# Performance work log

Measured on AMD Instinct MI355X. Metric: run time of the kernel, lower is better.

The kernel has to match this reference:

```python
import jax, jax.numpy as jnp
import numpy as np

N_WAY = 64

def setup_inputs() -> dict:
    key = jax.random.key(0)
    k1, k2, k3, k4 = jax.random.split(key, 4)
    S, Q, F, D = 1024, 16384, 2048, 512
    xs = jax.random.normal(k1, (S, F), dtype=jnp.float32)
    ys = jax.random.randint(k2, (S,), 0, N_WAY, dtype=jnp.int64)
    xq = jax.random.normal(k3, (Q, F), dtype=jnp.float32)
    W = jax.random.normal(k4, (F, D), dtype=jnp.float32) * 0.02
    b = jnp.zeros((D,), dtype=jnp.float32)
    return {"xs": xs, "ys": ys, "xq": xq, "W": W, "b": b}

def reference(xs, ys, xq, W, b):
    # encoder: linear projection [*, F] -> [*, D]
    z_s = xs @ W + b            # [S, D]
    z_q = xq @ W + b            # [Q, D]
    # class prototypes: segment mean over support embeddings -> [N_way, D]
    counts = jax.ops.segment_sum(jnp.ones_like(ys, dtype=z_s.dtype), ys, num_segments=N_WAY)
    proto = jax.ops.segment_sum(z_s, ys, num_segments=N_WAY) / jnp.clip(counts, 1.0)[:, None]
    # pairwise squared euclidean distance (expand + pow + sum), [Q, N_way]
    diff = z_q[:, None, :] - proto[None, :, :]   # [Q, N_way, D]
    dists = jnp.sum(diff * diff, axis=-1)
    return -dists
```

## Files before the change

### kernel.cpp

```cpp
#include <hip/hip_runtime.h>


typedef __attribute__((ext_vector_type(8))) short short8;
typedef __attribute__((ext_vector_type(4))) float floatx4;

#define S_ROWS 1024
#define F_DIM  2048
#define D_DIM  512
#define NWAY   64
#define Q_ROWS 16384
#define ZS_LD  136

static __device__ __forceinline__ unsigned short f2bf(float f) {
  unsigned int u = __float_as_uint(f);
  u += 0x7FFF + ((u >> 16) & 1);
  return (unsigned short)(u >> 16);
}
static __device__ __forceinline__ float bf2f(unsigned short s) {
  return __uint_as_float(((unsigned int)s) << 16);
}
static __device__ __forceinline__ unsigned int pack_bf2(float x, float y) {
  unsigned int ux = __float_as_uint(x) + 0x8000u;
  unsigned int uy = __float_as_uint(y) + 0x8000u;
  return __builtin_amdgcn_perm(uy, ux, 0x07060302u);
}
static __device__ __forceinline__ void load_lds16(const unsigned short* g, unsigned short* l) {
  __builtin_amdgcn_global_load_lds((const __attribute__((address_space(1))) unsigned int*)g,
                                   (__attribute__((address_space(3))) unsigned int*)l,
                                   16, 0, 0);
}

__global__ __launch_bounds__(256) void k_prep(const float* __restrict__ W,
                                              unsigned short* __restrict__ Wt,
                                              float* __restrict__ outz,
                                              float* __restrict__ pnorm_part,
                                              const int* __restrict__ ys,
                                              int* __restrict__ order,
                                              int* __restrict__ starts,
                                              float* __restrict__ counts) {
  __shared__ unsigned short t[64][65];
  __shared__ int cnt[NWAY];
  __shared__ int st[NWAY + 1];
  __shared__ int wp[NWAY];
  int bx = blockIdx.x;
  int tid = threadIdx.x;
  if (bx < 256) {
    float4 zz = {0.f, 0.f, 0.f, 0.f};
#pragma unroll
    for (int p = 0; p < 4; p++)
      *(float4*)&outz[(size_t)bx * 4096 + p * 1024 + tid * 4] = zz;
    int f0 = (bx >> 3) << 6;
    int d0 = (bx & 7) << 6;
    for (int j = 0; j < 16; j++) {
      int lin = j * 256 + tid;
      int fl = lin >> 6, dl = lin & 63;
      t[fl][dl] = f2bf(W[(size_t)(f0 + fl) * D_DIM + d0 + dl]);
    }
    __syncthreads();
    for (int j = 0; j < 16; j++) {
      int lin = j * 256 + tid;
      int dl = lin >> 6, fl = lin & 63;
      Wt[(size_t)(d0 + dl) * F_DIM + f0 + fl] = t[fl][dl];
    }
  } else {
    pnorm_part[tid] = 0.f;
    if (tid < NWAY) cnt[tid] = 0;
    __syncthreads();
    for (int j = tid; j < S_ROWS; j += 256) atomicAdd(&cnt[ys[j]], 1);
    __syncthreads();
    if (tid == 0) {
      int a = 0;
      for (int c = 0; c < NWAY; c++) { st[c] = a; wp[c] = a; a += cnt[c]; }
      st[NWAY] = a;
    }
    __syncthreads();
    for (int j = tid; j < S_ROWS; j += 256) {
      int c = ys[j];
      int p = atomicAdd(&wp[c], 1);
      order[p] = j;
    }
    if (tid < NWAY) counts[tid] = (float)cnt[tid];
    if (tid < NWAY + 1) starts[tid] = st[tid];
  }
}

__global__ __launch_bounds__(256) void k1_csum(const float* __restrict__ xs,
                                               const int* __restrict__ order,
                                               const int* __restrict__ starts,
                                               float* __restrict__ csum) {
  __shared__ int lord[S_ROWS];
  int c = blockIdx.x >> 1;
  int tid = threadIdx.x;
  int s = starts[c], e = starts[c + 1];
  int len = e - s;
  for (int j = tid; j < len; j += 256) lord[j] = order[s + j];
  __syncthreads();
  int f0 = (blockIdx.x & 1) * 1024 + tid * 4;
  float4 a = {0.f, 0.f, 0.f, 0.f};
  for (int i = 0; i < len; i++) {
    float4 v = *(const float4*)&xs[(size_t)lord[i] * F_DIM + f0];
    a.x += v.x; a.y += v.y; a.z += v.z; a.w += v.w;
  }
  *(float4*)&csum[(size_t)c * F_DIM + f0] = a;
}

__global__ __launch_bounds__(256) void k2_full(const float* __restrict__ W,
                                               const float* __restrict__ csum,
                                               const float* __restrict__ b,
                                               const float* __restrict__ counts,
                                               unsigned short* __restrict__ proto_bf,
                                               float* __restrict__ pnorm_part) {
  __shared__ __align__(16) float wch[64 * 64];
  __shared__ float csl[8 * 64];
  int bx = blockIdx.x;
  int cg = bx >> 3, dc = bx & 7;
  int c0 = cg * 8, d0 = dc * 64;
  int tid = threadIdx.x;
  int cl = tid >> 5;
  int dl = (tid & 31) * 2;
  float a0 = 0.f, a1 = 0.f;
  for (int fs = 0; fs < 32; fs++) {
    int f0 = fs * 64;
    __syncthreads();
    for (int idx = tid; idx < 4096; idx += 256) {
      int r = idx >> 6, q = idx & 63;
      wch[idx] = W[(size_t)(f0 + r) * D_DIM + d0 + q];
    }
    for (int idx = tid; idx < 512; idx += 256) {
      int r = idx >> 6, q = idx & 63;
      csl[idx] = csum[(size_t)(c0 + r) * F_DIM + f0 + q];
    }
    __syncthreads();
#pragma unroll 8
    for (int f = 0; f < 64; f++) {
      float s = csl[cl * 64 + f];
      a0 += s * wch[f * 64 + dl];
      a1 += s * wch[f * 64 + dl + 1];
    }
  }
  int c = c0 + cl;
  float cntv = counts[c];
  float inv = 1.f / fmaxf(cntv, 1.f);
  float p0 = (a0 + cntv * b[d0 + dl]) * inv;
  float p1 = (a1 + cntv * b[d0 + dl + 1]) * inv;
  unsigned short h0 = f2bf(p0), h1 = f2bf(p1);
  proto_bf[(size_t)c * D_DIM + d0 + dl] = h0;
  proto_bf[(size_t)c * D_DIM + d0 + dl + 1] = h1;
  float q0 = bf2f(h0), q1 = bf2f(h1);
  float s2 = q0 * q0 + q1 * q1;
  s2 += __shfl_xor(s2, 1, 32);
  s2 += __shfl_xor(s2, 2, 32);
  s2 += __shfl_xor(s2, 4, 32);
  s2 += __shfl_xor(s2, 8, 32);
  s2 += __shfl_xor(s2, 16, 32);
  if ((tid & 31) == 0) atomicAdd(&pnorm_part[(dc >> 1) * 64 + c], s2);
}

__global__ __launch_bounds__(256) void k3_fused(const float* __restrict__ xq,
                                                const unsigned short* __restrict__ Wt,
                                                const float* __restrict__ b,
                                                const unsigned short* __restrict__ proto_bf,
                                                const float* __restrict__ pnorm_part,
                                                float* __restrict__ out) {
  __shared__ __align__(16) char smem[66304];
  unsigned short* lA0 = (unsigned short*)smem;
  unsigned short* lB0 = (unsigned short*)(smem + 16384);
  unsigned short* lA1 = (unsigned short*)(smem + 32768);
  unsigned short* lB1 = (unsigned short*)(smem + 49152);
  unsigned short* zs = (unsigned short*)smem;
  float* qnf = (float*)(smem + 65536);
  float* pnl = (float*)(smem + 66048);

  int tid = threadIdx.x;
  int bx = blockIdx.x;
  int xcd = bx & 7;
  int wg = xcd * 64 + (bx >> 3);
  int mt = wg >> 2;
  int slice = wg & 3;
  int n0 = slice * 128;

  int wave = tid >> 6, lane = tid & 63;
  int wr = wave >> 1, wc = wave & 1;
  int lrow = lane & 15, lquad = lane >> 4;

  const float* Ab = xq + (size_t)mt * 128 * F_DIM;

  floatx4 acc[4][4];
#pragma unroll
  for (int i = 0; i < 4; i++)
#pragma unroll
    for (int j = 0; j < 4; j++) acc[i][j] = (floatx4){0.f, 0.f, 0.f, 0.f};

  int sr = tid >> 3, skq = tid & 7;
  const float* ag = Ab + (size_t)sr * F_DIM + skq * 8;
  const unsigned short* bg = Wt + (size_t)(n0 + sr) * F_DIM + skq * 8;

  float4 pf[4][2];

  auto stageB = [&](unsigned short* lBbuf, int k0) {
#pragma unroll
    for (int i = 0; i < 4; i++)
      load_lds16(bg + (size_t)i * 32 * F_DIM + k0, &lBbuf[(i * 256 + wave * 64) * 8]);
  };
  auto issueA = [&](int k0) {
#pragma unroll
    for (int p = 0; p < 4; p++) {
      const float* gp = ag + (size_t)p * 32 * F_DIM + k0;
      pf[p][0] = *(const float4*)gp;
      pf[p][1] = *(const float4*)(gp + 4);
    }
  };
  auto writeA = [&](unsigned short* lAbuf) {
#pragma unroll
    for (int p = 0; p < 4; p++) {
      uint4 w;
      w.x = pack_bf2(pf[p][0].x, pf[p][0].y);
      w.y = pack_bf2(pf[p][0].z, pf[p][0].w);
      w.z = pack_bf2(pf[p][1].x, pf[p][1].y);
      w.w = pack_bf2(pf[p][1].z, pf[p][1].w);
      *(uint4*)&lAbuf[(p * 256 + tid) * 8] = w;
    }
  };
  auto compute = [&](const unsigned short* lAbuf, const unsigned short* lBbuf) {
#pragma unroll
    for (int s = 0; s < 2; s++) {
      short8 af[4], bfr[4];
#pragma unroll
      for (int i = 0; i < 4; i++)
        af[i] = *(const short8*)&lAbuf[(wr * 64 + i * 16 + lrow) * 64 + s * 32 + lquad * 8];
#pragma unroll
      for (int j = 0; j < 4; j++)
        bfr[j] = *(const short8*)&lBbuf[(wc * 64 + j * 16 + lrow) * 64 + s * 32 + lquad * 8];
#pragma unroll
      for (int i = 0; i < 4; i++)
#pragma unroll
        for (int j = 0; j < 4; j++)
          acc[i][j] = __builtin_amdgcn_mfma_f32_16x16x32_bf16(af[i], bfr[j], acc[i][j], 0, 0, 0);
    }
  };

  stageB(lB0, 0);
  issueA(0);
  writeA(lA0);
  __syncthreads();

  for (int t = 0; t < 32; t += 2) {
    {
      int kn = (t + 1) * 64;
      stageB(lB1, kn);
      issueA(kn);
      compute(lA0, lB0);
      writeA(lA1);
      __syncthreads();
    }
    {
      if (t + 2 < 32) {
        int kn = (t + 2) * 64;
        stageB(lB0, kn);
        issueA(kn);
      }
      compute(lA1, lB1);
      if (t + 2 < 32) writeA(lA0);
      __syncthreads();
    }
  }

  if (tid < 128) qnf[tid] = 0.f;
  if (tid < 64) pnl[tid] = pnorm_part[slice * 64 + tid];
  __syncthreads();

#pragma unroll
  for (int i = 0; i < 4; i++) {
    float rn[4] = {0.f, 0.f, 0.f, 0.f};
#pragma unroll
    for (int j = 0; j < 4; j++) {
      int col = wc * 64 + j * 16 + lrow;
      float bb = b[n0 + col];
#pragma unroll
      for (int r = 0; r < 4; r++) {
        int row = wr * 64 + i * 16 + lquad * 4 + r;
        float v = acc[i][j][r] + bb;
        unsigned short h = f2bf(v);
        zs[row * ZS_LD + col] = h;
        float vq = bf2f(h);
        rn[r] += vq * vq;
      }
    }
#pragma unroll
    for (int r = 0; r < 4; r++) {
      float s2 = rn[r];
      s2 += __shfl_xor(s2, 1, 16);
      s2 += __shfl_xor(s2, 2, 16);
      s2 += __shfl_xor(s2, 4, 16);
      s2 += __shfl_xor(s2, 8, 16);
      if (lrow == 0) atomicAdd(&qnf[wr * 64 + i * 16 + lquad * 4 + r], s2);
    }
  }
  __syncthreads();

  floatx4 acc2[2][4];
#pragma unroll
  for (int i = 0; i < 2; i++)
#pragma unroll
    for (int j = 0; j < 4; j++) acc2[i][j] = (floatx4){0.f, 0.f, 0.f, 0.f};

#pragma unroll
  for (int ks = 0; ks < 4; ks++) {
    short8 af2[2], bp[4];
#pragma unroll
    for (int i = 0; i < 2; i++)
      af2[i] = *(const short8*)&zs[(wave * 32 + i * 16 + lrow) * ZS_LD + ks * 32 + lquad * 8];
#pragma unroll
    for (int j = 0; j < 4; j++)
      bp[j] = *(const short8*)&proto_bf[(size_t)(j * 16 + lrow) * D_DIM + n0 + ks * 32 + lquad * 8];
#pragma unroll
    for (int i = 0; i < 2; i++)
#pragma unroll
      for (int j = 0; j < 4; j++)
        acc2[i][j] = __builtin_amdgcn_mfma_f32_16x16x32_bf16(af2[i], bp[j], acc2[i][j], 0, 0, 0);
  }

  size_t qbase = (size_t)mt * 128;
#pragma unroll
  for (int i = 0; i < 2; i++) {
#pragma unroll
    for (int j = 0; j < 4; j++) {
      int c = j * 16 + lrow;
      float pn = pnl[c];
#pragma unroll
      for (int r = 0; r < 4; r++) {
        int ql = wave * 32 + i * 16 + lquad * 4 + r;
        float val = 2.f * acc2[i][j][r] - qnf[ql] - pn;
        atomicAdd(&out[(qbase + ql) * NWAY + c], val);
      }
    }
  }
}

extern "C" void kernel_launch(void* const* d_in, const int* in_sizes, int n_in,
                              void* d_out, int out_size, void* d_ws, size_t ws_size,
                              hipStream_t stream) {
  const float* xs = (const float*)d_in[0];
  const int* ys = (const int*)d_in[1];
  const float* xq = (const float*)d_in[2];
  const float* W = (const float*)d_in[3];
  const float* b = (const float*)d_in[4];
  float* out = (float*)d_out;
  char* ws = (char*)d_ws;

  size_t off = 0;
  auto take = [&](size_t bytes) -> char* {
    char* r = ws + off;
    off += (bytes + 255) & ~(size_t)255;
    return r;
  };
  unsigned short* Wt = (unsigned short*)take((size_t)D_DIM * F_DIM * 2);
  float* csum = (float*)take((size_t)NWAY * F_DIM * 4);
  unsigned short* proto_bf = (unsigned short*)take((size_t)NWAY * D_DIM * 2);
  float* counts = (float*)take(NWAY * 4);
  float* pnorm_part = (float*)take(4 * NWAY * 4);
  int* order = (int*)take(S_ROWS * 4);
  int* starts = (int*)take((NWAY + 1) * 4);

  if (off > ws_size) return;

  k_prep<<<257, 256, 0, stream>>>(W, Wt, out, pnorm_part, ys, order, starts, counts);
  k1_csum<<<128, 256, 0, stream>>>(xs, order, starts, csum);
  k2_full<<<64, 256, 0, stream>>>(W, csum, b, counts, proto_bf, pnorm_part);
  k3_fused<<<512, 256, 0, stream>>>(xq, Wt, b, proto_bf, pnorm_part, out);
}
```

Baseline: 326.4 us.

## Shrink fused GEMM tile to 64 rows, single-buffer LDS, raise occupancy

The fused query kernel moves from 128x128 tiles with double-buffered LDS and register-prefetched A to 64x128 tiles with a single LDS buffer, and the grid doubles to 1024 blocks. Launch bounds now request 4 blocks per CU, and the LDS footprint drops from about 66KB to about 25KB. The goal is to hide memory latency through more resident waves rather than software pipelining. In exchange, each block loads W slices for half as many rows, so B-operand global traffic doubles, and each k-step now needs two barriers with no overlap inside a block.

```diff
diff --git a/kernel.cpp b/kernel.cpp
--- a/kernel.cpp
+++ b/kernel.cpp
@@ -156,129 +156,94 @@
   if ((tid & 31) == 0) atomicAdd(&pnorm_part[(dc >> 1) * 64 + c], s2);
 }
 
-__global__ __launch_bounds__(256) void k3_fused(const float* __restrict__ xq,
-                                                const unsigned short* __restrict__ Wt,
-                                                const float* __restrict__ b,
-                                                const unsigned short* __restrict__ proto_bf,
-                                                const float* __restrict__ pnorm_part,
-                                                float* __restrict__ out) {
-  __shared__ __align__(16) char smem[66304];
-  unsigned short* lA0 = (unsigned short*)smem;
-  unsigned short* lB0 = (unsigned short*)(smem + 16384);
-  unsigned short* lA1 = (unsigned short*)(smem + 32768);
-  unsigned short* lB1 = (unsigned short*)(smem + 49152);
+__global__ __launch_bounds__(256, 4) void k3_fused(const float* __restrict__ xq,
+                                                   const unsigned short* __restrict__ Wt,
+                                                   const float* __restrict__ b,
+                                                   const unsigned short* __restrict__ proto_bf,
+                                                   const float* __restrict__ pnorm_part,
+                                                   float* __restrict__ out) {
+  __shared__ __align__(16) char smem[25088];
+  unsigned short* lA = (unsigned short*)smem;
+  unsigned short* lB = (unsigned short*)(smem + 8192);
   unsigned short* zs = (unsigned short*)smem;
-  float* qnf = (float*)(smem + 65536);
-  float* pnl = (float*)(smem + 66048);
+  float* qnf = (float*)(smem + 24576);
+  float* pnl = (float*)(smem + 24832);
 
   int tid = threadIdx.x;
   int bx = blockIdx.x;
   int xcd = bx & 7;
-  int wg = xcd * 64 + (bx >> 3);
+  int wg = xcd * 128 + (bx >> 3);
   int mt = wg >> 2;
   int slice = wg & 3;
   int n0 = slice * 128;
 
   int wave = tid >> 6, lane = tid & 63;
-  int wr = wave >> 1, wc = wave & 1;
+  int wm = wave >> 1, wn = wave & 1;
   int lrow = lane & 15, lquad = lane >> 4;
 
-  const float* Ab = xq + (size_t)mt * 128 * F_DIM;
-
-  floatx4 acc[4][4];
-#pragma unroll
-  for (int i = 0; i < 4; i++)
+  const float* Ab = xq + (size_t)mt * 64 * F_DIM;
+
+  floatx4 acc[2][4];
+#pragma unroll
+  for (int i = 0; i < 2; i++)
 #pragma unroll
     for (int j = 0; j < 4; j++) acc[i][j] = (floatx4){0.f, 0.f, 0.f, 0.f};
 
-  int sr = tid >> 3, skq = tid & 7;
-  const float* ag = Ab + (size_t)sr * F_DIM + skq * 8;
-  const unsigned short* bg = Wt + (size_t)(n0 + sr) * F_DIM + skq * 8;
-
-  float4 pf[4][2];
-
-  auto stageB = [&](unsigned short* lBbuf, int k0) {
+  int arow = tid >> 2, akq = tid & 3;
+  const float* ag = Ab + (size_t)arow * F_DIM + akq * 16;
+  unsigned short* aw = &lA[arow * 64 + akq * 16];
+  const unsigned short* bg = Wt + (size_t)(n0 + (tid >> 3)) * F_DIM + (tid & 7) * 8;
+
+  for (int k0 = 0; k0 < F_DIM; k0 += 64) {
 #pragma unroll
     for (int i = 0; i < 4; i++)
-      load_lds16(bg + (size_t)i * 32 * F_DIM + k0, &lBbuf[(i * 256 + wave * 64) * 8]);
-  };
-  auto issueA = [&](int k0) {
-#pragma unroll
-    for (int p = 0; p < 4; p++) {
-      const float* gp = ag + (size_t)p * 32 * F_DIM + k0;
-      pf[p][0] = *(const float4*)gp;
-      pf[p][1] = *(const float4*)(gp + 4);
-    }
-  };
-  auto writeA = [&](unsigned short* lAbuf) {
-#pragma unroll
-    for (int p = 0; p < 4; p++) {
-      uint4 w;
-      w.x = pack_bf2(pf[p][0].x, pf[p][0].y);
-      w.y = pack_bf2(pf[p][0].z, pf[p][0].w);
-      w.z = pack_bf2(pf[p][1].x, pf[p][1].y);
-      w.w = pack_bf2(pf[p][1].z, pf[p][1].w);
-      *(uint4*)&lAbuf[(p * 256 + tid) * 8] = w;
-    }
-  };
-  auto compute = [&](const unsigned short* lAbuf, const unsigned short* lBbuf) {
+      load_lds16(bg + (size_t)i * 32 * F_DIM + k0, &lB[(i * 256 + wave * 64) * 8]);
+    {
+      const float* gp = ag + k0;
+      float4 v0 = *(const float4*)gp;
+      float4 v1 = *(const float4*)(gp + 4);
+      float4 v2 = *(const float4*)(gp + 8);
+      float4 v3 = *(const float4*)(gp + 12);
+      uint4 w0, w1;
+      w0.x = pack_bf2(v0.x, v0.y); w0.y = pack_bf2(v0.z, v0.w);
+      w0.z = pack_bf2(v1.x, v1.y); w0.w = pack_bf2(v1.z, v1.w);
+      w1.x = pack_bf2(v2.x, v2.y); w1.y = pack_bf2(v2.z, v2.w);
+      w1.z = pack_bf2(v3.x, v3.y); w1.w = pack_bf2(v3.z, v3.w);
+      *(uint4*)aw = w0;
+      *(uint4*)(aw + 8) = w1;
+    }
+    __syncthreads();
 #pragma unroll
     for (int s = 0; s < 2; s++) {
-      short8 af[4], bfr[4];
-#pragma unroll
-      for (int i = 0; i < 4; i++)
-        af[i] = *(const short8*)&lAbuf[(wr * 64 + i * 16 + lrow) * 64 + s * 32 + lquad * 8];
+      short8 af[2], bfr[4];
+#pragma unroll
+      for (int i = 0; i < 2; i++)
+        af[i] = *(const short8*)&lA[(wm * 32 + i * 16 + lrow) * 64 + s * 32 + lquad * 8];
 #pragma unroll
       for (int j = 0; j < 4; j++)
-        bfr[j] = *(const short8*)&lBbuf[(wc * 64 + j * 16 + lrow) * 64 + s * 32 + lquad * 8];
-#pragma unroll
-      for (int i = 0; i < 4; i++)
+        bfr[j] = *(const short8*)&lB[(wn * 64 + j * 16 + lrow) * 64 + s * 32 + lquad * 8];
+#pragma unroll
+      for (int i = 0; i < 2; i++)
 #pragma unroll
         for (int j = 0; j < 4; j++)
           acc[i][j] = __builtin_amdgcn_mfma_f32_16x16x32_bf16(af[i], bfr[j], acc[i][j], 0, 0, 0);
     }
-  };
-
-  stageB(lB0, 0);
-  issueA(0);
-  writeA(lA0);
+    __syncthreads();
+  }
+
+  if (tid < 64) { qnf[tid] = 0.f; pnl[tid] = pnorm_part[slice * 64 + tid]; }
   __syncthreads();
 
-  for (int t = 0; t < 32; t += 2) {
-    {
-      int kn = (t + 1) * 64;
-      stageB(lB1, kn);
-      issueA(kn);
-      compute(lA0, lB0);
-      writeA(lA1);
-      __syncthreads();
-    }
-    {
-      if (t + 2 < 32) {
-        int kn = (t + 2) * 64;
-        stageB(lB0, kn);
-        issueA(kn);
-      }
-      compute(lA1, lB1);
-      if (t + 2 < 32) writeA(lA0);
-      __syncthreads();
-    }
-  }
-
-  if (tid < 128) qnf[tid] = 0.f;
-  if (tid < 64) pnl[tid] = pnorm_part[slice * 64 + tid];
-  __syncthreads();
-
-#pragma unroll
-  for (int i = 0; i < 4; i++) {
+#pragma unroll
+  for (int i = 0; i < 2; i++) {
     float rn[4] = {0.f, 0.f, 0.f, 0.f};
 #pragma unroll
     for (int j = 0; j < 4; j++) {
-      int col = wc * 64 + j * 16 + lrow;
+      int col = wn * 64 + j * 16 + lrow;
       float bb = b[n0 + col];
 #pragma unroll
       for (int r = 0; r < 4; r++) {
-        int row = wr * 64 + i * 16 + lquad * 4 + r;
+        int row = wm * 32 + i * 16 + lquad * 4 + r;
         float v = acc[i][j][r] + bb;
         unsigned short h = f2bf(v);
         zs[row * ZS_LD + col] = h;
@@ -293,46 +258,35 @@
       s2 += __shfl_xor(s2, 2, 16);
       s2 += __shfl_xor(s2, 4, 16);
       s2 += __shfl_xor(s2, 8, 16);
-      if (lrow == 0) atomicAdd(&qnf[wr * 64 + i * 16 + lquad * 4 + r], s2);
+      if (lrow == 0) atomicAdd(&qnf[wm * 32 + i * 16 + lquad * 4 + r], s2);
     }
   }
   __syncthreads();
 
-  floatx4 acc2[2][4];
-#pragma unroll
-  for (int i = 0; i < 2; i++)
-#pragma unroll
-    for (int j = 0; j < 4; j++) acc2[i][j] = (floatx4){0.f, 0.f, 0.f, 0.f};
+  floatx4 acc2[4];
+#pragma unroll
+  for (int j = 0; j < 4; j++) acc2[j] = (floatx4){0.f, 0.f, 0.f, 0.f};
 
 #pragma unroll
   for (int ks = 0; ks < 4; ks++) {
-    short8 af2[2], bp[4];
-#pragma unroll
-    for (int i = 0; i < 2; i++)
-      af2[i] = *(const short8*)&zs[(wave * 32 + i * 16 + lrow) * ZS_LD + ks * 32 + lquad * 8];
-#pragma unroll
-    for (int j = 0; j < 4; j++)
-      bp[j] = *(const short8*)&proto_bf[(size_t)(j * 16 + lrow) * D_DIM + n0 + ks * 32 + lquad * 8];
-#pragma unroll
-    for (int i = 0; i < 2; i++)
-#pragma unroll
-      for (int j = 0; j < 4; j++)
-        acc2[i][j] = __builtin_amdgcn_mfma_f32_16x16x32_bf16(af2[i], bp[j], acc2[i][j], 0, 0, 0);
-  }
-
-  size_t qbase = (size_t)mt * 128;
-#pragma unroll
-  for (int i = 0; i < 2; i++) {
+    short8 af2 = *(const short8*)&zs[(wave * 16 + lrow) * ZS_LD + ks * 32 + lquad * 8];
 #pragma unroll
     for (int j = 0; j < 4; j++) {
-      int c = j * 16 + lrow;
-      float pn = pnl[c];
-#pragma unroll
-      for (int r = 0; r < 4; r++) {
-        int ql = wave * 32 + i * 16 + lquad * 4 + r;
-        float val = 2.f * acc2[i][j][r] - qnf[ql] - pn;
-        atomicAdd(&out[(qbase + ql) * NWAY + c], val);
-      }
+      short8 bp = *(const short8*)&proto_bf[(size_t)(j * 16 + lrow) * D_DIM + n0 + ks * 32 + lquad * 8];
+      acc2[j] = __builtin_amdgcn_mfma_f32_16x16x32_bf16(af2, bp, acc2[j], 0, 0, 0);
+    }
+  }
+
+  size_t qbase = (size_t)mt * 64;
+#pragma unroll
+  for (int j = 0; j < 4; j++) {
+    int c = j * 16 + lrow;
+    float pn = pnl[c];
+#pragma unroll
+    for (int r = 0; r < 4; r++) {
+      int ql = wave * 16 + lquad * 4 + r;
+      float val = 2.f * acc2[j][r] - qnf[ql] - pn;
+      atomicAdd(&out[(qbase + ql) * NWAY + c], val);
     }
   }
 }
@@ -367,5 +321,5 @@
   k_prep<<<257, 256, 0, stream>>>(W, Wt, out, pnorm_part, ys, order, starts, counts);
   k1_csum<<<128, 256, 0, stream>>>(xs, order, starts, csum);
   k2_full<<<64, 256, 0, stream>>>(W, csum, b, counts, proto_bf, pnorm_part);
-  k3_fused<<<512, 256, 0, stream>>>(xq, Wt, b, proto_bf, pnorm_part, out);
-}
+  k3_fused<<<1024, 256, 0, stream>>>(xq, Wt, b, proto_bf, pnorm_part, out);
+}
```

Result: slower. 347.1 us (+6.3%).

## Pre-convert xq to bf16 and stream A tiles via direct LDS loads

Applied to the files above, without the earlier changes.

Adds a pass in the prep kernel that converts the query matrix to bf16 in workspace, so the fused GEMM kernel can load A tiles with global-to-LDS DMA instead of register loads plus packing. The GEMM main loop is restructured to a single-buffered K=128 step, replacing the previous double-buffered K=64 pipeline. This halves the per-slice A read size but adds a full conversion pass over xq and removes load/compute overlap. A fallback keeps the fp32 path when the workspace is too small.

```diff
diff --git a/kernel.cpp b/kernel.cpp
--- a/kernel.cpp
+++ b/kernel.cpp
@@ -37,13 +37,28 @@
                                               const int* __restrict__ ys,
                                               int* __restrict__ order,
                                               int* __restrict__ starts,
-                                              float* __restrict__ counts) {
+                                              float* __restrict__ counts,
+                                              const float* __restrict__ xq,
+                                              unsigned short* __restrict__ xqb) {
   __shared__ unsigned short t[64][65];
   __shared__ int cnt[NWAY];
   __shared__ int st[NWAY + 1];
   __shared__ int wp[NWAY];
   int bx = blockIdx.x;
   int tid = threadIdx.x;
+  if (bx >= 257) {
+    size_t base = (size_t)(bx - 257) * 8192 + (size_t)tid * 32;
+#pragma unroll
+    for (int u = 0; u < 4; u++) {
+      float4 v0 = *(const float4*)&xq[base + u * 8];
+      float4 v1 = *(const float4*)&xq[base + u * 8 + 4];
+      uint4 w;
+      w.x = pack_bf2(v0.x, v0.y); w.y = pack_bf2(v0.z, v0.w);
+      w.z = pack_bf2(v1.x, v1.y); w.w = pack_bf2(v1.z, v1.w);
+      *(uint4*)&xqb[base + u * 8] = w;
+    }
+    return;
+  }
   if (bx < 256) {
     float4 zz = {0.f, 0.f, 0.f, 0.f};
 #pragma unroll
@@ -156,17 +171,17 @@
   if ((tid & 31) == 0) atomicAdd(&pnorm_part[(dc >> 1) * 64 + c], s2);
 }
 
+template <int ADMA>
 __global__ __launch_bounds__(256) void k3_fused(const float* __restrict__ xq,
+                                                const unsigned short* __restrict__ xqb,
                                                 const unsigned short* __restrict__ Wt,
                                                 const float* __restrict__ b,
                                                 const unsigned short* __restrict__ proto_bf,
                                                 const float* __restrict__ pnorm_part,
                                                 float* __restrict__ out) {
   __shared__ __align__(16) char smem[66304];
-  unsigned short* lA0 = (unsigned short*)smem;
-  unsigned short* lB0 = (unsigned short*)(smem + 16384);
-  unsigned short* lA1 = (unsigned short*)(smem + 32768);
-  unsigned short* lB1 = (unsigned short*)(smem + 49152);
+  unsigned short* lA = (unsigned short*)smem;
+  unsigned short* lB = (unsigned short*)(smem + 32768);
   unsigned short* zs = (unsigned short*)smem;
   float* qnf = (float*)(smem + 65536);
   float* pnl = (float*)(smem + 66048);
@@ -178,91 +193,62 @@
   int mt = wg >> 2;
   int slice = wg & 3;
   int n0 = slice * 128;
+  int m0 = mt * 128;
 
   int wave = tid >> 6, lane = tid & 63;
   int wr = wave >> 1, wc = wave & 1;
   int lrow = lane & 15, lquad = lane >> 4;
 
-  const float* Ab = xq + (size_t)mt * 128 * F_DIM;
-
   floatx4 acc[4][4];
 #pragma unroll
   for (int i = 0; i < 4; i++)
 #pragma unroll
     for (int j = 0; j < 4; j++) acc[i][j] = (floatx4){0.f, 0.f, 0.f, 0.f};
 
-  int sr = tid >> 3, skq = tid & 7;
-  const float* ag = Ab + (size_t)sr * F_DIM + skq * 8;
-  const unsigned short* bg = Wt + (size_t)(n0 + sr) * F_DIM + skq * 8;
-
-  float4 pf[4][2];
-
-  auto stageB = [&](unsigned short* lBbuf, int k0) {
-#pragma unroll
-    for (int i = 0; i < 4; i++)
-      load_lds16(bg + (size_t)i * 32 * F_DIM + k0, &lBbuf[(i * 256 + wave * 64) * 8]);
-  };
-  auto issueA = [&](int k0) {
-#pragma unroll
-    for (int p = 0; p < 4; p++) {
-      const float* gp = ag + (size_t)p * 32 * F_DIM + k0;
-      pf[p][0] = *(const float4*)gp;
-      pf[p][1] = *(const float4*)(gp + 4);
-    }
-  };
-  auto writeA = [&](unsigned short* lAbuf) {
-#pragma unroll
-    for (int p = 0; p < 4; p++) {
-      uint4 w;
-      w.x = pack_bf2(pf[p][0].x, pf[p][0].y);
-      w.y = pack_bf2(pf[p][0].z, pf[p][0].w);
-      w.z = pack_bf2(pf[p][1].x, pf[p][1].y);
-      w.w = pack_bf2(pf[p][1].z, pf[p][1].w);
-      *(uint4*)&lAbuf[(p * 256 + tid) * 8] = w;
-    }
-  };
-  auto compute = [&](const unsigned short* lAbuf, const unsigned short* lBbuf) {
-#pragma unroll
-    for (int s = 0; s < 2; s++) {
+  int srow = tid >> 4, scolq = tid & 15;
+  const unsigned short* ag =
+      ADMA ? xqb + (size_t)(m0 + srow) * F_DIM + scolq * 8 : (const unsigned short*)0;
+  const unsigned short* bg = Wt + (size_t)(n0 + srow) * F_DIM + scolq * 8;
+  const float* agf =
+      ADMA ? (const float*)0 : xq + (size_t)(m0 + srow) * F_DIM + scolq * 8;
+
+  for (int k0 = 0; k0 < F_DIM; k0 += 128) {
+#pragma unroll
+    for (int i = 0; i < 8; i++)
+      load_lds16(bg + (size_t)i * 16 * F_DIM + k0, &lB[(i * 256 + wave * 64) * 8]);
+    if constexpr (ADMA) {
+#pragma unroll
+      for (int i = 0; i < 8; i++)
+        load_lds16(ag + (size_t)i * 16 * F_DIM + k0, &lA[(i * 256 + wave * 64) * 8]);
+    } else {
+#pragma unroll
+      for (int p = 0; p < 8; p++) {
+        const float* gp = agf + (size_t)p * 16 * F_DIM + k0;
+        float4 v0 = *(const float4*)gp;
+        float4 v1 = *(const float4*)(gp + 4);
+        uint4 w;
+        w.x = pack_bf2(v0.x, v0.y); w.y = pack_bf2(v0.z, v0.w);
+        w.z = pack_bf2(v1.x, v1.y); w.w = pack_bf2(v1.z, v1.w);
+        *(uint4*)&lA[(p * 256 + tid) * 8] = w;
+      }
+    }
+    __syncthreads();
+#pragma unroll
+    for (int s = 0; s < 4; s++) {
       short8 af[4], bfr[4];
 #pragma unroll
       for (int i = 0; i < 4; i++)
-        af[i] = *(const short8*)&lAbuf[(wr * 64 + i * 16 + lrow) * 64 + s * 32 + lquad * 8];
+        af[i] = *(const short8*)&lA[(wr * 64 + i * 16 + lrow) * 128 + s * 32 + lquad * 8];
 #pragma unroll
       for (int j = 0; j < 4; j++)
-        bfr[j] = *(const short8*)&lBbuf[(wc * 64 + j * 16 + lrow) * 64 + s * 32 + lquad * 8];
+        bfr[j] = *(const short8*)&lB[(wc * 64 + j * 16 + lrow) * 128 + s * 32 + lquad * 8];
 #pragma unroll
       for (int i = 0; i < 4; i++)
 #pragma unroll
         for (int j = 0; j < 4; j++)
           acc[i][j] = __builtin_amdgcn_mfma_f32_16x16x32_bf16(af[i], bfr[j], acc[i][j], 0, 0, 0);
     }
-  };
-
-  stageB(lB0, 0);
-  issueA(0);
-  writeA(lA0);
-  __syncthreads();
-
-  for (int t = 0; t < 32; t += 2) {
-    {
-      int kn = (t + 1) * 64;
-      stageB(lB1, kn);
-      issueA(kn);
-      compute(lA0, lB0);
-      writeA(lA1);
-      __syncthreads();
-    }
-    {
-      if (t + 2 < 32) {
-        int kn = (t + 2) * 64;
-        stageB(lB0, kn);
-        issueA(kn);
-      }
-      compute(lA1, lB1);
-      if (t + 2 < 32) writeA(lA0);
-      __syncthreads();
-    }
+    __syncthreads();
   }
 
   if (tid < 128) qnf[tid] = 0.f;
@@ -361,11 +347,24 @@
   float* pnorm_part = (float*)take(4 * NWAY * 4);
   int* order = (int*)take(S_ROWS * 4);
   int* starts = (int*)take((NWAY + 1) * 4);
-
-  if (off > ws_size) return;
-
-  k_prep<<<257, 256, 0, stream>>>(W, Wt, out, pnorm_part, ys, order, starts, counts);
+  size_t base_off = off;
+  unsigned short* xqb = (unsigned short*)take((size_t)Q_ROWS * F_DIM * 2);
+
+  if (base_off > ws_size) return;
+  bool adma = (off <= ws_size);
+
+  if (adma) {
+    k_prep<<<257 + 4096, 256, 0, stream>>>(W, Wt, out, pnorm_part, ys, order,
+                                           starts, counts, xq, xqb);
+  } else {
+    k_prep<<<257, 256, 0, stream>>>(W, Wt, out, pnorm_part, ys, order,
+                                    starts, counts, xq, (unsigned short*)0);
+  }
   k1_csum<<<128, 256, 0, stream>>>(xs, order, starts, csum);
   k2_full<<<64, 256, 0, stream>>>(W, csum, b, counts, proto_bf, pnorm_part);
-  k3_fused<<<512, 256, 0, stream>>>(xq, Wt, b, proto_bf, pnorm_part, out);
-}
+  if (adma) {
+    k3_fused<1><<<512, 256, 0, stream>>>(xq, xqb, Wt, b, proto_bf, pnorm_part, out);
+  } else {
+    k3_fused<0><<<512, 256, 0, stream>>>(xq, xqb, Wt, b, proto_bf, pnorm_part, out);
+  }
+}
```

New measurement: 382.7 us. 17.3% more time.

## Deepen B prefetch to 4-stage ring, swizzle LDS, and use fine-grained waitcnt barriers

Applied to the files above, without the earlier changes.

The k3 main GEMM loop now stages B tiles two steps ahead into a four-buffer LDS ring, while A keeps a double buffer. It uses explicit vmcnt/lgkmcnt waits with raw s_barrier in place of __syncthreads, so async global->LDS loads can stay in flight across the barrier. An XOR swizzle on the 16-byte column chunk is meant to cut LDS bank conflicts on the MFMA fragment reads, and s_setprio raises priority around the MFMA block. LDS use grows to about 97KB, which may lower occupancy, and the hand-written waitcnt counts must match the issued loads or results go wrong.

```diff
diff --git a/kernel.cpp b/kernel.cpp
--- a/kernel.cpp
+++ b/kernel.cpp
@@ -10,6 +10,7 @@
 #define NWAY   64
 #define Q_ROWS 16384
 #define ZS_LD  136
+#define NSTEP  32
 
 static __device__ __forceinline__ unsigned short f2bf(float f) {
   unsigned int u = __float_as_uint(f);
@@ -162,14 +163,12 @@
                                                 const unsigned short* __restrict__ proto_bf,
                                                 const float* __restrict__ pnorm_part,
                                                 float* __restrict__ out) {
-  __shared__ __align__(16) char smem[66304];
-  unsigned short* lA0 = (unsigned short*)smem;
-  unsigned short* lB0 = (unsigned short*)(smem + 16384);
-  unsigned short* lA1 = (unsigned short*)(smem + 32768);
-  unsigned short* lB1 = (unsigned short*)(smem + 49152);
-  unsigned short* zs = (unsigned short*)smem;
-  float* qnf = (float*)(smem + 65536);
-  float* pnl = (float*)(smem + 66048);
+  __shared__ __align__(16) char smem[99072];
+  unsigned short* lA = (unsigned short*)smem;
+  unsigned short* lB = (unsigned short*)(smem + 32768);
+  unsigned short* zs = (unsigned short*)(smem + 32768);
+  float* qnf = (float*)(smem + 98304);
+  float* pnl = (float*)(smem + 98816);
 
   int tid = threadIdx.x;
   int bx = blockIdx.x;
@@ -178,12 +177,12 @@
   int mt = wg >> 2;
   int slice = wg & 3;
   int n0 = slice * 128;
+  int m0 = mt * 128;
 
   int wave = tid >> 6, lane = tid & 63;
   int wr = wave >> 1, wc = wave & 1;
   int lrow = lane & 15, lquad = lane >> 4;
-
-  const float* Ab = xq + (size_t)mt * 128 * F_DIM;
+  int rsw = lrow & 7;
 
   floatx4 acc[4][4];
 #pragma unroll
@@ -191,80 +190,86 @@
 #pragma unroll
     for (int j = 0; j < 4; j++) acc[i][j] = (floatx4){0.f, 0.f, 0.f, 0.f};
 
-  int sr = tid >> 3, skq = tid & 7;
-  const float* ag = Ab + (size_t)sr * F_DIM + skq * 8;
-  const unsigned short* bg = Wt + (size_t)(n0 + sr) * F_DIM + skq * 8;
+  int srow = tid >> 3;
+  int skq = tid & 7;
+  int sswz = srow & 7;
+  const float* ag = xq + (size_t)(m0 + srow) * F_DIM + skq * 8;
+  const unsigned short* bg = Wt + (size_t)(n0 + srow) * F_DIM + (skq ^ sswz) * 8;
 
   float4 pf[4][2];
 
-  auto stageB = [&](unsigned short* lBbuf, int k0) {
-#pragma unroll
-    for (int i = 0; i < 4; i++)
-      load_lds16(bg + (size_t)i * 32 * F_DIM + k0, &lBbuf[(i * 256 + wave * 64) * 8]);
-  };
-  auto issueA = [&](int k0) {
-#pragma unroll
-    for (int p = 0; p < 4; p++) {
-      const float* gp = ag + (size_t)p * 32 * F_DIM + k0;
-      pf[p][0] = *(const float4*)gp;
-      pf[p][1] = *(const float4*)(gp + 4);
-    }
-  };
-  auto writeA = [&](unsigned short* lAbuf) {
-#pragma unroll
-    for (int p = 0; p < 4; p++) {
-      uint4 w;
-      w.x = pack_bf2(pf[p][0].x, pf[p][0].y);
-      w.y = pack_bf2(pf[p][0].z, pf[p][0].w);
-      w.z = pack_bf2(pf[p][1].x, pf[p][1].y);
-      w.w = pack_bf2(pf[p][1].z, pf[p][1].w);
-      *(uint4*)&lAbuf[(p * 256 + tid) * 8] = w;
-    }
-  };
-  auto compute = [&](const unsigned short* lAbuf, const unsigned short* lBbuf) {
-#pragma unroll
-    for (int s = 0; s < 2; s++) {
-      short8 af[4], bfr[4];
-#pragma unroll
-      for (int i = 0; i < 4; i++)
-        af[i] = *(const short8*)&lAbuf[(wr * 64 + i * 16 + lrow) * 64 + s * 32 + lquad * 8];
-#pragma unroll
-      for (int j = 0; j < 4; j++)
-        bfr[j] = *(const short8*)&lBbuf[(wc * 64 + j * 16 + lrow) * 64 + s * 32 + lquad * 8];
-#pragma unroll
-      for (int i = 0; i < 4; i++)
-#pragma unroll
-        for (int j = 0; j < 4; j++)
-          acc[i][j] = __builtin_amdgcn_mfma_f32_16x16x32_bf16(af[i], bfr[j], acc[i][j], 0, 0, 0);
-    }
-  };
-
-  stageB(lB0, 0);
-  issueA(0);
-  writeA(lA0);
+#define STAGE_B(kstep, buf)                                                     \
+  {                                                                             \
+    _Pragma("unroll") for (int i_ = 0; i_ < 4; i_++)                            \
+        load_lds16(bg + (size_t)i_ * 32 * F_DIM + (kstep) * 64,                 \
+                   &lB[(size_t)(buf) * 8192 + (i_ * 256 + wave * 64) * 8]);     \
+  }
+#define ISSUE_A(kstep)                                                          \
+  {                                                                             \
+    _Pragma("unroll") for (int p_ = 0; p_ < 4; p_++) {                          \
+      const float* gp_ = ag + (size_t)p_ * 32 * F_DIM + (kstep) * 64;           \
+      pf[p_][0] = *(const float4*)gp_;                                          \
+      pf[p_][1] = *(const float4*)(gp_ + 4);                                    \
+    }                                                                           \
+  }
+#define WRITE_A(buf)                                                            \
+  {                                                                             \
+    _Pragma("unroll") for (int p_ = 0; p_ < 4; p_++) {                          \
+      uint4 w_;                                                                 \
+      w_.x = pack_bf2(pf[p_][0].x, pf[p_][0].y);                                \
+      w_.y = pack_bf2(pf[p_][0].z, pf[p_][0].w);                                \
+      w_.z = pack_bf2(pf[p_][1].x, pf[p_][1].y);                                \
+      w_.w = pack_bf2(pf[p_][1].z, pf[p_][1].w);                                \
+      *(uint4*)&lA[(size_t)(buf) * 8192 + ((p_ * 32 + srow) * 64 +              \
+                                           ((skq ^ sswz) * 8))] = w_;           \
+    }                                                                           \
+  }
+#define COMPUTE(ca, cb)                                                         \
+  {                                                                             \
+    _Pragma("unroll") for (int s_ = 0; s_ < 2; s_++) {                          \
+      short8 af_[4], bf_[4];                                                    \
+      int cx_ = ((s_ * 4 + lquad) ^ rsw) * 8;                                   \
+      _Pragma("unroll") for (int i_ = 0; i_ < 4; i_++)                          \
+          af_[i_] = *(const short8*)&lA[(size_t)(ca) * 8192 +                   \
+                                        (wr * 64 + i_ * 16 + lrow) * 64 + cx_]; \
+      _Pragma("unroll") for (int j_ = 0; j_ < 4; j_++)                          \
+          bf_[j_] = *(const short8*)&lB[(size_t)(cb) * 8192 +                   \
+                                        (wc * 64 + j_ * 16 + lrow) * 64 + cx_]; \
+      __builtin_amdgcn_s_setprio(1);                                            \
+      _Pragma("unroll") for (int i_ = 0; i_ < 4; i_++)                          \
+          _Pragma("unroll") for (int j_ = 0; j_ < 4; j_++)                      \
+              acc[i_][j_] = __builtin_amdgcn_mfma_f32_16x16x32_bf16(            \
+                  af_[i_], bf_[j_], acc[i_][j_], 0, 0, 0);                      \
+      __builtin_amdgcn_s_setprio(0);                                            \
+    }                                                                           \
+  }
+
+  STAGE_B(0, 0);
+  ISSUE_A(0);
+  WRITE_A(0);
+  STAGE_B(1, 1);
+  asm volatile("s_waitcnt lgkmcnt(0)" ::: "memory");
+  asm volatile("s_waitcnt vmcnt(4)" ::: "memory");
+  __builtin_amdgcn_s_barrier();
+  __builtin_amdgcn_sched_barrier(0);
+
+  for (int t = 0; t < NSTEP; ++t) {
+    int cb = t & 3, ca = t & 1;
+    if (t + 2 < NSTEP) STAGE_B(t + 2, (t + 2) & 3);
+    if (t + 1 < NSTEP) ISSUE_A(t + 1);
+    COMPUTE(ca, cb);
+    if (t + 1 < NSTEP) WRITE_A((t + 1) & 1);
+    asm volatile("s_waitcnt lgkmcnt(0)" ::: "memory");
+    if (t + 2 < NSTEP) {
+      asm volatile("s_waitcnt vmcnt(4)" ::: "memory");
+    } else {
+      asm volatile("s_waitcnt vmcnt(0)" ::: "memory");
+    }
+    __builtin_amdgcn_s_barrier();
+    __builtin_amdgcn_sched_barrier(0);
+  }
+
   __syncthreads();
-
-  for (int t = 0; t < 32; t += 2) {
-    {
-      int kn = (t + 1) * 64;
-      stageB(lB1, kn);
-      issueA(kn);
-      compute(lA0, lB0);
-      writeA(lA1);
-      __syncthreads();
-    }
-    {
-      if (t + 2 < 32) {
-        int kn = (t + 2) * 64;
-        stageB(lB0, kn);
-        issueA(kn);
-      }
-      compute(lA1, lB1);
-      if (t + 2 < 32) writeA(lA0);
-      __syncthreads();
-    }
-  }
-
   if (tid < 128) qnf[tid] = 0.f;
   if (tid < 64) pnl[tid] = pnorm_part[slice * 64 + tid];
   __syncthreads();
```

Result: slower. 360.7 us (+10.5%).
